# Kernel tuning notes

Hardware: AMD Instinct MI355X
Metric: run time of the kernel (lower is better)

Reference implementation:

```python
import jax, jax.numpy as jnp
import numpy as np

N = 100000      # nodes
E = 1600000     # edges
F_IN = 512      # num_features
H = 128         # hidden
C = 40          # num_classes
K = 10          # Chebyshev order


def setup_inputs() -> dict:
    key = jax.random.key(0)
    ks = jax.random.split(key, 6)
    x = jax.random.normal(ks[0], (N, F_IN), dtype=jnp.float32)
    edge_index = jax.random.randint(ks[1], (2, E), 0, N, dtype=jnp.int32)
    W1 = jax.random.normal(ks[2], (F_IN, H), dtype=jnp.float32) / np.sqrt(F_IN).astype(np.float32)
    b1 = jnp.zeros((H,), dtype=jnp.float32)
    W2 = jax.random.normal(ks[3], (H, C), dtype=jnp.float32) / np.sqrt(H).astype(np.float32)
    b2 = jnp.zeros((C,), dtype=jnp.float32)
    # Chebyshev coefficients temp[K+1]
    temp = 1.0 + 0.1 * jax.random.normal(ks[4], (K + 1,), dtype=jnp.float32)
    return {"x": x, "edge_index": edge_index, "W1": W1, "b1": b1, "W2": W2, "b2": b2, "temp": temp}


def reference(x, edge_index, W1, b1, W2, b2, temp):
    # MLP encoder (eval mode: dropout is identity)
    h = jax.nn.relu(x @ W1 + b1)          # [N, H]
    h = h @ W2 + b2                        # [N, C]

    # gcn_norm: add self-loops, symmetric normalization
    self_loop = jnp.arange(N, dtype=edge_index.dtype)
    row = jnp.concatenate([edge_index[0], self_loop])   # [E+N]
    col = jnp.concatenate([edge_index[1], self_loop])
    deg = jax.ops.segment_sum(jnp.ones_like(row, dtype=jnp.float32), row, num_segments=N)
    dis = jnp.where(deg > 0, jax.lax.rsqrt(jnp.maximum(deg, 1.0)), 0.0)
    norm = dis[row] * dis[col]             # [E+N]

    def prop(v):  # A_hat @ v : gather-scale-scatter over edges
        return jax.ops.segment_sum(norm[:, None] * v[col], row, num_segments=N)

    # Chebyshev recurrence: Tx_k = 2*A_hat*Tx_{k-1} - Tx_{k-2}
    Tx0 = h
    Tx1 = prop(h)
    out0 = temp[0] * Tx0 + temp[1] * Tx1

    def body(carry, coe):
        t0, t1, acc = carry
        t2 = 2.0 * prop(t1) - t0
        return (t1, t2, acc + coe * t2), None

    (_, _, out), _ = jax.lax.scan(body, (Tx0, Tx1, out0), temp[2:])
    return jax.nn.log_softmax(out, axis=1)
```

## Files before the change

### kernel.cpp

```cpp
#include <hip/hip_runtime.h>
#include <hip/hip_bf16.h>
#include <cstdint>
#include <cstddef>

#define NN   100000
#define EE   1600000
#define FIN  512
#define HID  128
#define CC   40
#define KORD 10
#define SHB  80
#define SHSTRIDE ((size_t)NN * SHB)

typedef __attribute__((ext_vector_type(4))) float f4;
typedef __attribute__((ext_vector_type(8))) short short8_t;
typedef __attribute__((ext_vector_type(4))) unsigned int u4;
typedef __attribute__((ext_vector_type(4), aligned(4))) int i4u;

__device__ __forceinline__ unsigned short cvt_bf16(float f) {
  union { float f; unsigned u; } a; a.f = f;
  unsigned r = a.u + 0x7fffu + ((a.u >> 16) & 1u);
  return (unsigned short)(r >> 16);
}
__device__ __forceinline__ unsigned pk_bf(float a, float b) {
  union { float f; unsigned u; } x, y; x.f = a; y.f = b;
  unsigned ra = x.u + 0x7fffu + ((x.u >> 16) & 1u);
  unsigned rb = y.u + 0x7fffu + ((y.u >> 16) & 1u);
  return (ra >> 16) | (rb & 0xffff0000u);
}
__device__ __forceinline__ unsigned pk_tr(float a, float b) {
  union { float f; unsigned u; } x, y; x.f = a; y.f = b;
  return (x.u >> 16) | (y.u & 0xffff0000u);
}
__device__ __forceinline__ f4 cvf2(unsigned lo, unsigned hi) {
  union { unsigned u; float f; } a, b, c, d;
  a.u = lo << 16; b.u = lo & 0xffff0000u;
  c.u = hi << 16; d.u = hi & 0xffff0000u;
  f4 r; r.x = a.f; r.y = b.f; r.z = c.f; r.w = d.f; return r;
}

__global__ __launch_bounds__(256) void k_dw(const int* __restrict__ rowI, int* __restrict__ deg,
                                            const float* __restrict__ W1, unsigned short* __restrict__ W1T,
                                            int ndeg) {
  int b = blockIdx.x;
  if (b < ndeg) {
    int i = b * 256 + threadIdx.x;
    if (i < EE) atomicAdd(&deg[rowI[i]], 1);
  } else {
    int idx = (b - ndeg) * 256 + threadIdx.x;
    int k = idx >> 7, n = idx & 127;
    W1T[(k >> 5) * 4096 + n * 32 + (k & 31)] = cvt_bf16(W1[idx]);
  }
}

__global__ __launch_bounds__(256) void k_scan1(const int* __restrict__ cnt, int* __restrict__ excl,
                                               int* __restrict__ bsums) {
  __shared__ int s[256];
  int tid = threadIdx.x;
  int base = blockIdx.x * 1024 + tid * 4;
  int v0 = (base + 0 < NN) ? cnt[base + 0] + 1 : 0;
  int v1 = (base + 1 < NN) ? cnt[base + 1] + 1 : 0;
  int v2 = (base + 2 < NN) ? cnt[base + 2] + 1 : 0;
  int v3 = (base + 3 < NN) ? cnt[base + 3] + 1 : 0;
  int tsum = v0 + v1 + v2 + v3;
  s[tid] = tsum;
  __syncthreads();
  for (int off = 1; off < 256; off <<= 1) {
    int t = (tid >= off) ? s[tid - off] : 0;
    __syncthreads();
    if (tid >= off) s[tid] += t;
    __syncthreads();
  }
  int run = s[tid] - tsum;
  if (tid == 255) bsums[blockIdx.x] = s[255];
  if (base + 0 < NN) excl[base + 0] = run; run += v0;
  if (base + 1 < NN) excl[base + 1] = run; run += v1;
  if (base + 2 < NN) excl[base + 2] = run; run += v2;
  if (base + 3 < NN) excl[base + 3] = run;
}

__global__ __launch_bounds__(128) void k_scan2(int* __restrict__ bsums, int nb) {
  __shared__ int s[128];
  int tid = threadIdx.x;
  int v = (tid < nb) ? bsums[tid] : 0;
  s[tid] = v;
  __syncthreads();
  for (int off = 1; off < 128; off <<= 1) {
    int t = (tid >= off) ? s[tid - off] : 0;
    __syncthreads();
    if (tid >= off) s[tid] += t;
    __syncthreads();
  }
  if (tid < nb) bsums[tid] = s[tid] - v;
}

__global__ __launch_bounds__(256) void k_scan3(const int* __restrict__ cnt, int* __restrict__ rs,
                                               int* __restrict__ cur, const int* __restrict__ bsums,
                                               float* __restrict__ dis, float* __restrict__ sqd,
                                               float* __restrict__ invd) {
  int i = blockIdx.x * 256 + threadIdx.x;
  if (i < NN) {
    int v = rs[i] + bsums[i >> 10];
    rs[i] = v;
    cur[i] = v;
    int d = cnt[i] + 1;
    if (i == NN - 1) rs[NN] = v + d;
    float fd = (float)d;
    dis[i]  = rsqrtf(fd);
    sqd[i]  = sqrtf(fd);
    invd[i] = 1.0f / fd;
  }
}

#define SLICE_ROWS (NN / 8)
#define SC_CHUNK   2048
__global__ __launch_bounds__(256) void k_scatter(const int* __restrict__ rowI, const int* __restrict__ colI,
                                                 int* __restrict__ cur, int* __restrict__ colS) {
  int slice = blockIdx.x & 7;
  int chunk = blockIdx.x >> 3;
  int lo = slice * SLICE_ROWS, hi = lo + SLICE_ROWS;
#pragma unroll
  for (int t = 0; t < SC_CHUNK / 256; ++t) {
    int i = chunk * SC_CHUNK + t * 256 + threadIdx.x;
    if (i < EE + NN) {
      int r = (i < EE) ? rowI[i] : (i - EE);
      if (r >= lo && r < hi) {
        int c = (i < EE) ? colI[i] : r;
        int pos = atomicAdd(&cur[r], 1);
        colS[pos] = c * SHB;
      }
    }
  }
}

#define LDK 40
__global__ __launch_bounds__(256) void k_gemm1(const float* __restrict__ x, const unsigned short* __restrict__ W1T,
                                               const float* __restrict__ b1, float* __restrict__ h1) {
  __shared__ __align__(16) float As_f[128 * 32];
  __shared__ __align__(16) short Bs_s[128][LDK];
  int tid  = threadIdx.x;
  int wave = tid >> 6, lane = tid & 63;
  int blockRow = blockIdx.x * 128;
  int wr = (wave & 1) * 64, wc = (wave >> 1) * 64;
  int l15 = lane & 15, hi4 = lane >> 4;

  int sr = (wave << 5) + (lane >> 3);
  int sslot = lane & 7;

  f4 acc[4][4] = {};

  for (int k0 = 0; k0 < FIN; k0 += 32) {
#pragma unroll
    for (int c = 0; c < 4; ++c) {
      int row = sr + c * 8;
      int gr = blockRow + row;
      int lslot = sslot ^ (row & 7);
      const float* gp = x + (size_t)gr * FIN + k0 + lslot * 4;
      float* lp = &As_f[(wave << 10) + (c << 8)];
      if (gr < NN) {
        __builtin_amdgcn_global_load_lds(
            (const __attribute__((address_space(1))) unsigned int*)gp,
            (__attribute__((address_space(3))) unsigned int*)lp, 16, 0, 0);
      }
    }

    const unsigned short* Wt = W1T + (k0 >> 5) * 4096;
    short8_t q0 = *(const short8_t*)&Wt[tid * 16];
    short8_t q1 = *(const short8_t*)&Wt[tid * 16 + 8];
    int bn = tid >> 1, bkk = (tid & 1) * 16;
    *(short8_t*)&Bs_s[bn][bkk]     = q0;
    *(short8_t*)&Bs_s[bn][bkk + 8] = q1;

    __syncthreads();

    short8_t afr[4], bfr[4];
#pragma unroll
    for (int m = 0; m < 4; ++m) {
      int row = wr + m * 16 + l15;
      int s0 = (hi4 * 2) ^ (row & 7);
      int s1 = (hi4 * 2 + 1) ^ (row & 7);
      f4 a0 = *(const f4*)&As_f[(row << 5) + s0 * 4];
      f4 a1 = *(const f4*)&As_f[(row << 5) + s1 * 4];
      u4 p;
      p.x = pk_tr(a0.x, a0.y); p.y = pk_tr(a0.z, a0.w);
      p.z = pk_tr(a1.x, a1.y); p.w = pk_tr(a1.z, a1.w);
      afr[m] = *(short8_t*)&p;
    }
#pragma unroll
    for (int n = 0; n < 4; ++n) bfr[n] = *(const short8_t*)&Bs_s[wc + n * 16 + l15][hi4 * 8];
#pragma unroll
    for (int m = 0; m < 4; ++m)
#pragma unroll
      for (int n = 0; n < 4; ++n)
        acc[m][n] = __builtin_amdgcn_mfma_f32_16x16x32_bf16(afr[m], bfr[n], acc[m][n], 0, 0, 0);

    __syncthreads();
  }

  float bias[4];
#pragma unroll
  for (int n = 0; n < 4; ++n) bias[n] = b1[wc + n * 16 + l15];
#pragma unroll
  for (int m = 0; m < 4; ++m) {
    int baseRow = blockRow + wr + m * 16 + hi4 * 4;
#pragma unroll
    for (int n = 0; n < 4; ++n) {
      int col = wc + n * 16 + l15;
#pragma unroll
      for (int r = 0; r < 4; ++r) {
        int grow = baseRow + r;
        if (grow < NN) h1[(size_t)grow * HID + col] = fmaxf(acc[m][n][r] + bias[n], 0.f);
      }
    }
  }
}

__global__ __launch_bounds__(256) void k_gemm2(const float* __restrict__ h1, const float* __restrict__ W2,
                                               const float* __restrict__ b2, const float* __restrict__ temp,
                                               const float* __restrict__ dis,
                                               unsigned short* __restrict__ sh0) {
  __shared__ float sW[HID * CC];
  __shared__ float sb[CC];
  int tid = threadIdx.x;
  for (int i = tid; i < HID * CC; i += 256) sW[i] = W2[i];
  if (tid < CC) sb[tid] = b2[tid];
  __syncthreads();
  int gid = blockIdx.x * 256 + tid;
  if (gid >= NN * 20) return;
  int row = gid / 20;
  int c2  = (gid - row * 20) * 2;
  const float* hr = h1 + (size_t)row * HID;
  float a0 = sb[c2], a1 = sb[c2 + 1];
#pragma unroll 8
  for (int k = 0; k < HID; ++k) {
    float hv = hr[k];
    a0 = fmaf(hv, sW[k * CC + c2], a0);
    a1 = fmaf(hv, sW[k * CC + c2 + 1], a1);
  }
  float dv = dis[row];
  *(unsigned*)((char*)sh0 + (size_t)row * SHB + c2 * 2) = pk_bf(a0 * dv, a1 * dv);
}

template <int MODE>
__global__ __launch_bounds__(256, 8) void k_prop(const unsigned short* __restrict__ shIn,
                                                 const unsigned short* __restrict__ shPrev,
                                                 unsigned short* __restrict__ shOut,
                                                 const int* __restrict__ colS,
                                                 const int* __restrict__ rs,
                                                 const float* __restrict__ invd) {
  int lane = threadIdx.x & 63;
  int wave = threadIdx.x >> 6;
  int grp  = lane / 5;
  int fi   = lane - grp * 5;
  int node = blockIdx.x * 48 + wave * 12 + grp;
  bool active = (grp < 12) && (node < NN);
  int s = 0, e = 0;
  if (active) { s = rs[node]; e = rs[node + 1]; }
  const char* base = (const char*)shIn + fi * 16;
  f4 z = {0.f, 0.f, 0.f, 0.f};
  f4 alo0 = z, ahi0 = z, alo1 = z, ahi1 = z;
  int j = s;
  for (; j + 4 <= e; j += 4) {
    i4u c = *(const i4u*)&colS[j];
    u4 p0 = *(const u4*)(base + c.x);
    u4 p1 = *(const u4*)(base + c.y);
    u4 p2 = *(const u4*)(base + c.z);
    u4 p3 = *(const u4*)(base + c.w);
    alo0 += cvf2(p0.x, p0.y); ahi0 += cvf2(p0.z, p0.w);
    alo1 += cvf2(p1.x, p1.y); ahi1 += cvf2(p1.z, p1.w);
    alo0 += cvf2(p2.x, p2.y); ahi0 += cvf2(p2.z, p2.w);
    alo1 += cvf2(p3.x, p3.y); ahi1 += cvf2(p3.z, p3.w);
  }
  if (j + 2 <= e) {
    u4 p0 = *(const u4*)(base + colS[j]);
    u4 p1 = *(const u4*)(base + colS[j + 1]);
    alo0 += cvf2(p0.x, p0.y); ahi0 += cvf2(p0.z, p0.w);
    alo1 += cvf2(p1.x, p1.y); ahi1 += cvf2(p1.z, p1.w);
    j += 2;
  }
  if (j < e) {
    u4 p0 = *(const u4*)(base + colS[j]);
    alo0 += cvf2(p0.x, p0.y); ahi0 += cvf2(p0.z, p0.w);
  }

  if (active) {
    f4 slo = alo0 + alo1;
    f4 shi = ahi0 + ahi1;
    float iv = invd[node];
    size_t ro = (size_t)node * SHB + fi * 16;
    f4 wlo, whi;
    if (MODE == 0) {
      wlo = iv * slo; whi = iv * shi;
    } else {
      u4 pp = __builtin_nontemporal_load((const u4*)((const char*)shPrev + ro));
      f4 plo = cvf2(pp.x, pp.y), phi = cvf2(pp.z, pp.w);
      wlo = (2.f * iv) * slo - plo;
      whi = (2.f * iv) * shi - phi;
    }
    u4 pk;
    pk.x = pk_bf(wlo.x, wlo.y); pk.y = pk_bf(wlo.z, wlo.w);
    pk.z = pk_bf(whi.x, whi.y); pk.w = pk_bf(whi.z, whi.w);
    *(u4*)((char*)shOut + ro) = pk;
  }
}

__global__ __launch_bounds__(256) void k_comb(const unsigned short* __restrict__ shBase,
                                              float* __restrict__ outF,
                                              const float* __restrict__ sqd,
                                              const float* __restrict__ temp) {
  int lane = threadIdx.x & 63;
  int wave = threadIdx.x >> 6;
  int grp  = lane / 5;
  int fi   = lane - grp * 5;
  int node = blockIdx.x * 48 + wave * 12 + grp;
  if (grp >= 12 || node >= NN) return;

  const char* p = (const char*)shBase + (size_t)node * SHB + fi * 16;
  f4 alo = {0.f,0.f,0.f,0.f}, ahi = alo;
#pragma unroll
  for (int k = 0; k <= KORD; ++k) {
    u4 pp = *(const u4*)(p + (size_t)k * SHSTRIDE);
    float tk = temp[k];
    alo += tk * cvf2(pp.x, pp.y);
    ahi += tk * cvf2(pp.z, pp.w);
  }
  float sq = sqd[node];
  alo *= sq; ahi *= sq;

  int gb = grp * 5;
  float m = fmaxf(fmaxf(fmaxf(alo.x, alo.y), fmaxf(alo.z, alo.w)),
                  fmaxf(fmaxf(ahi.x, ahi.y), fmaxf(ahi.z, ahi.w)));
  float mm = m;
#pragma unroll
  for (int j = 0; j < 5; ++j) mm = fmaxf(mm, __shfl(m, gb + j));
  float ss = expf(alo.x - mm) + expf(alo.y - mm) + expf(alo.z - mm) + expf(alo.w - mm)
           + expf(ahi.x - mm) + expf(ahi.y - mm) + expf(ahi.z - mm) + expf(ahi.w - mm);
  float tot = 0.f;
#pragma unroll
  for (int j = 0; j < 5; ++j) tot += __shfl(ss, gb + j);
  float lse = mm + logf(tot);
  alo -= lse; ahi -= lse;
  size_t o = (size_t)node * CC + fi * 8;
  *(f4*)&outF[o]     = alo;
  *(f4*)&outF[o + 4] = ahi;
}

extern "C" void kernel_launch(void* const* d_in, const int* in_sizes, int n_in,
                              void* d_out, int out_size, void* d_ws, size_t ws_size,
                              hipStream_t stream) {
  const float* x    = (const float*)d_in[0];
  const int*   ei   = (const int*)d_in[1];
  const float* W1   = (const float*)d_in[2];
  const float* b1   = (const float*)d_in[3];
  const float* W2   = (const float*)d_in[4];
  const float* b2   = (const float*)d_in[5];
  const float* temp = (const float*)d_in[6];
  const int* rowI = ei;
  const int* colI = ei + EE;
  float* out = (float*)d_out;

  char* w = (char*)d_ws;
  auto alloc = [&](size_t bytes) -> void* {
    void* p = (void*)w;
    w += (bytes + 255) & ~(size_t)255;
    return p;
  };
  int*   deg   = (int*)  alloc((size_t)NN * 4);
  float* dis   = (float*)alloc((size_t)NN * 4);
  float* sqd   = (float*)alloc((size_t)NN * 4);
  float* invd  = (float*)alloc((size_t)NN * 4);
  int*   rs    = (int*)  alloc((size_t)(NN + 1) * 4);
  int*   cur   = (int*)  alloc((size_t)NN * 4);
  int*   bsums = (int*)  alloc(512 * 4);
  unsigned short* W1T = (unsigned short*)alloc((size_t)FIN * HID * 2);
  unsigned short* shAll = (unsigned short*)alloc(SHSTRIDE * (KORD + 1));
  int*   colS  = (int*)  alloc((size_t)(EE + NN) * 4);
  float* h1    = (float*)alloc((size_t)NN * HID * 4);

  auto sh = [&](int k) -> unsigned short* {
    return (unsigned short*)((char*)shAll + (size_t)k * SHSTRIDE);
  };

  hipMemsetAsync(deg, 0, (size_t)NN * 4, stream);

  const int NDEG = (EE + 255) / 256;
  const int NW1T = FIN * HID / 256;
  k_dw<<<NDEG + NW1T, 256, 0, stream>>>(rowI, deg, W1, W1T, NDEG);

  int nb = (NN + 1023) / 1024;
  k_scan1<<<nb, 256, 0, stream>>>(deg, rs, bsums);
  k_scan2<<<1, 128, 0, stream>>>(bsums, nb);
  k_scan3<<<(NN + 255) / 256, 256, 0, stream>>>(deg, rs, cur, bsums, dis, sqd, invd);

  const int NCH = (EE + NN + SC_CHUNK - 1) / SC_CHUNK;
  k_scatter<<<8 * NCH, 256, 0, stream>>>(rowI, colI, cur, colS);

  k_gemm1<<<(NN + 127) / 128, 256, 0, stream>>>(x, W1T, b1, h1);
  k_gemm2<<<(NN * 20 + 255) / 256, 256, 0, stream>>>(h1, W2, b2, temp, dis, sh(0));

  int G = (NN + 47) / 48;
  k_prop<0><<<G, 256, 0, stream>>>(sh(0), sh(0), sh(1), colS, rs, invd);
  for (int k = 2; k <= KORD; ++k) {
    k_prop<1><<<G, 256, 0, stream>>>(sh(k - 1), sh(k - 2), sh(k), colS, rs, invd);
  }

  k_comb<<<(NN + 47) / 48, 256, 0, stream>>>(shAll, out, sqd, temp);
}
```

Measured before the change: 631.9 us.

## Sort nodes by degree for load-balanced propagation and pad feature rows

Adds a degree histogram and counting sort that builds a permutation of nodes ordered by degree. The propagation kernels then process nodes in this order, so the groups within a wave have similar edge counts and lanes sit idle less. The per-node feature stride also grows from 80 to 128 bytes, which aligns rows but raises memory footprint and gather traffic. Node processing order becomes scattered, which may hurt write locality.

```diff
diff --git a/kernel.cpp b/kernel.cpp
--- a/kernel.cpp
+++ b/kernel.cpp
@@ -9,7 +9,7 @@
 #define HID  128
 #define CC   40
 #define KORD 10
-#define SHB  80
+#define SHB  128
 #define SHSTRIDE ((size_t)NN * SHB)
 
 typedef __attribute__((ext_vector_type(4))) float f4;
@@ -54,14 +54,18 @@
 }
 
 __global__ __launch_bounds__(256) void k_scan1(const int* __restrict__ cnt, int* __restrict__ excl,
-                                               int* __restrict__ bsums) {
+                                               int* __restrict__ bsums, int* __restrict__ hist) {
   __shared__ int s[256];
+  __shared__ int lh[256];
   int tid = threadIdx.x;
+  lh[tid] = 0;
+  __syncthreads();
   int base = blockIdx.x * 1024 + tid * 4;
-  int v0 = (base + 0 < NN) ? cnt[base + 0] + 1 : 0;
-  int v1 = (base + 1 < NN) ? cnt[base + 1] + 1 : 0;
-  int v2 = (base + 2 < NN) ? cnt[base + 2] + 1 : 0;
-  int v3 = (base + 3 < NN) ? cnt[base + 3] + 1 : 0;
+  int v0 = 0, v1 = 0, v2 = 0, v3 = 0;
+  if (base + 0 < NN) { v0 = cnt[base + 0] + 1; atomicAdd(&lh[min(v0, 255)], 1); }
+  if (base + 1 < NN) { v1 = cnt[base + 1] + 1; atomicAdd(&lh[min(v1, 255)], 1); }
+  if (base + 2 < NN) { v2 = cnt[base + 2] + 1; atomicAdd(&lh[min(v2, 255)], 1); }
+  if (base + 3 < NN) { v3 = cnt[base + 3] + 1; atomicAdd(&lh[min(v3, 255)], 1); }
   int tsum = v0 + v1 + v2 + v3;
   s[tid] = tsum;
   __syncthreads();
@@ -77,38 +81,63 @@
   if (base + 1 < NN) excl[base + 1] = run; run += v1;
   if (base + 2 < NN) excl[base + 2] = run; run += v2;
   if (base + 3 < NN) excl[base + 3] = run;
-}
-
-__global__ __launch_bounds__(128) void k_scan2(int* __restrict__ bsums, int nb) {
-  __shared__ int s[128];
+  if (lh[tid] > 0) atomicAdd(&hist[tid], lh[tid]);
+}
+
+__global__ __launch_bounds__(256) void k_scan2h(int* __restrict__ bsums, int nb, int* __restrict__ hist) {
+  __shared__ int s[256];
   int tid = threadIdx.x;
-  int v = (tid < nb) ? bsums[tid] : 0;
+  int* arr = (blockIdx.x == 0) ? bsums : hist;
+  int lim  = (blockIdx.x == 0) ? nb : 256;
+  int v = (tid < lim) ? arr[tid] : 0;
   s[tid] = v;
   __syncthreads();
-  for (int off = 1; off < 128; off <<= 1) {
+  for (int off = 1; off < 256; off <<= 1) {
     int t = (tid >= off) ? s[tid - off] : 0;
     __syncthreads();
     if (tid >= off) s[tid] += t;
     __syncthreads();
   }
-  if (tid < nb) bsums[tid] = s[tid] - v;
-}
-
-__global__ __launch_bounds__(256) void k_scan3(const int* __restrict__ cnt, int* __restrict__ rs,
-                                               int* __restrict__ cur, const int* __restrict__ bsums,
-                                               float* __restrict__ dis, float* __restrict__ sqd,
-                                               float* __restrict__ invd) {
-  int i = blockIdx.x * 256 + threadIdx.x;
-  if (i < NN) {
-    int v = rs[i] + bsums[i >> 10];
-    rs[i] = v;
-    cur[i] = v;
-    int d = cnt[i] + 1;
-    if (i == NN - 1) rs[NN] = v + d;
-    float fd = (float)d;
-    dis[i]  = rsqrtf(fd);
-    sqd[i]  = sqrtf(fd);
-    invd[i] = 1.0f / fd;
+  if (tid < lim) arr[tid] = s[tid] - v;
+}
+
+__global__ __launch_bounds__(256) void k_scan3p(const int* __restrict__ cnt, int* __restrict__ rs,
+                                                int* __restrict__ cur, const int* __restrict__ bsums,
+                                                float* __restrict__ dis, float* __restrict__ sqd,
+                                                float* __restrict__ invd,
+                                                const int* __restrict__ hoff, int* __restrict__ gcur,
+                                                int* __restrict__ perm, int nb3) {
+  int b = blockIdx.x;
+  int tid = threadIdx.x;
+  if (b < nb3) {
+    int i = b * 256 + tid;
+    if (i < NN) {
+      int v = rs[i] + bsums[i >> 10];
+      rs[i] = v;
+      cur[i] = v;
+      int d = cnt[i] + 1;
+      if (i == NN - 1) rs[NN] = v + d;
+      float fd = (float)d;
+      dis[i]  = rsqrtf(fd);
+      sqd[i]  = sqrtf(fd);
+      invd[i] = 1.0f / fd;
+    }
+  } else {
+    __shared__ int lh[256];
+    __shared__ int lb[256];
+    lh[tid] = 0;
+    __syncthreads();
+    int i = (b - nb3) * 256 + tid;
+    int d = 0, rank = 0;
+    bool ok = (i < NN);
+    if (ok) {
+      d = min(cnt[i] + 1, 255);
+      rank = atomicAdd(&lh[d], 1);
+    }
+    __syncthreads();
+    if (lh[tid] > 0) lb[tid] = atomicAdd(&gcur[tid], lh[tid]);
+    __syncthreads();
+    if (ok) perm[hoff[d] + lb[d] + rank] = i;
   }
 }
 
@@ -247,15 +276,16 @@
                                                  unsigned short* __restrict__ shOut,
                                                  const int* __restrict__ colS,
                                                  const int* __restrict__ rs,
+                                                 const int* __restrict__ perm,
                                                  const float* __restrict__ invd) {
   int lane = threadIdx.x & 63;
   int wave = threadIdx.x >> 6;
   int grp  = lane / 5;
   int fi   = lane - grp * 5;
-  int node = blockIdx.x * 48 + wave * 12 + grp;
-  bool active = (grp < 12) && (node < NN);
-  int s = 0, e = 0;
-  if (active) { s = rs[node]; e = rs[node + 1]; }
+  int nidx = blockIdx.x * 48 + wave * 12 + grp;
+  bool active = (grp < 12) && (nidx < NN);
+  int node = 0, s = 0, e = 0;
+  if (active) { node = perm[nidx]; s = rs[node]; e = rs[node + 1]; }
   const char* base = (const char*)shIn + fi * 16;
   f4 z = {0.f, 0.f, 0.f, 0.f};
   f4 alo0 = z, ahi0 = z, alo1 = z, ahi1 = z;
@@ -371,7 +401,10 @@
   float* invd  = (float*)alloc((size_t)NN * 4);
   int*   rs    = (int*)  alloc((size_t)(NN + 1) * 4);
   int*   cur   = (int*)  alloc((size_t)NN * 4);
+  int*   perm  = (int*)  alloc((size_t)NN * 4);
   int*   bsums = (int*)  alloc(512 * 4);
+  int*   hist  = (int*)  alloc(256 * 4);
+  int*   gcur  = (int*)  alloc(256 * 4);
   unsigned short* W1T = (unsigned short*)alloc((size_t)FIN * HID * 2);
   unsigned short* shAll = (unsigned short*)alloc(SHSTRIDE * (KORD + 1));
   int*   colS  = (int*)  alloc((size_t)(EE + NN) * 4);
@@ -382,15 +415,18 @@
   };
 
   hipMemsetAsync(deg, 0, (size_t)NN * 4, stream);
+  hipMemsetAsync(hist, 0, 256 * 4, stream);
+  hipMemsetAsync(gcur, 0, 256 * 4, stream);
 
   const int NDEG = (EE + 255) / 256;
   const int NW1T = FIN * HID / 256;
   k_dw<<<NDEG + NW1T, 256, 0, stream>>>(rowI, deg, W1, W1T, NDEG);
 
   int nb = (NN + 1023) / 1024;
-  k_scan1<<<nb, 256, 0, stream>>>(deg, rs, bsums);
-  k_scan2<<<1, 128, 0, stream>>>(bsums, nb);
-  k_scan3<<<(NN + 255) / 256, 256, 0, stream>>>(deg, rs, cur, bsums, dis, sqd, invd);
+  k_scan1<<<nb, 256, 0, stream>>>(deg, rs, bsums, hist);
+  k_scan2h<<<2, 256, 0, stream>>>(bsums, nb, hist);
+  int nb3 = (NN + 255) / 256;
+  k_scan3p<<<2 * nb3, 256, 0, stream>>>(deg, rs, cur, bsums, dis, sqd, invd, hist, gcur, perm, nb3);
 
   const int NCH = (EE + NN + SC_CHUNK - 1) / SC_CHUNK;
   k_scatter<<<8 * NCH, 256, 0, stream>>>(rowI, colI, cur, colS);
@@ -399,9 +435,9 @@
   k_gemm2<<<(NN * 20 + 255) / 256, 256, 0, stream>>>(h1, W2, b2, temp, dis, sh(0));
 
   int G = (NN + 47) / 48;
-  k_prop<0><<<G, 256, 0, stream>>>(sh(0), sh(0), sh(1), colS, rs, invd);
+  k_prop<0><<<G, 256, 0, stream>>>(sh(0), sh(0), sh(1), colS, rs, perm, invd);
   for (int k = 2; k <= KORD; ++k) {
-    k_prop<1><<<G, 256, 0, stream>>>(sh(k - 1), sh(k - 2), sh(k), colS, rs, invd);
+    k_prop<1><<<G, 256, 0, stream>>>(sh(k - 1), sh(k - 2), sh(k), colS, rs, perm, invd);
   }
 
   k_comb<<<(NN + 47) / 48, 256, 0, stream>>>(shAll, out, sqd, temp);
```

Result: slower. 678.1 us (+7.3%).

## Split propagation features into two column halves with separate node-major planes

Applied to the files above, without the earlier changes.

Stores each Chebyshev feature buffer as two 40-byte-per-node planes (first and second 20 classes) instead of one 80-byte row, and launches the propagation kernel over both halves with twice the blocks. Each half-plane is 4 MB instead of 8 MB, so the working set of the random gathers in each half-pass is smaller and more likely to stay cache-resident. Each gather becomes an 8-byte load instead of 16 bytes. In exchange, the edge list and row pointers are read twice per propagation step, and more, smaller memory transactions are issued.

```diff
diff --git a/kernel.cpp b/kernel.cpp
--- a/kernel.cpp
+++ b/kernel.cpp
@@ -9,12 +9,13 @@
 #define HID  128
 #define CC   40
 #define KORD 10
-#define SHB  80
-#define SHSTRIDE ((size_t)NN * SHB)
+#define HBYTES ((size_t)NN * 40)
+#define SHSTRIDE ((size_t)NN * 80)
 
 typedef __attribute__((ext_vector_type(4))) float f4;
 typedef __attribute__((ext_vector_type(8))) short short8_t;
 typedef __attribute__((ext_vector_type(4))) unsigned int u4;
+typedef __attribute__((ext_vector_type(2))) unsigned int u2;
 typedef __attribute__((ext_vector_type(4), aligned(4))) int i4u;
 
 __device__ __forceinline__ unsigned short cvt_bf16(float f) {
@@ -127,7 +128,7 @@
       if (r >= lo && r < hi) {
         int c = (i < EE) ? colI[i] : r;
         int pos = atomicAdd(&cur[r], 1);
-        colS[pos] = c * SHB;
+        colS[pos] = c * 40;
       }
     }
   }
@@ -238,7 +239,9 @@
     a1 = fmaf(hv, sW[k * CC + c2 + 1], a1);
   }
   float dv = dis[row];
-  *(unsigned*)((char*)sh0 + (size_t)row * SHB + c2 * 2) = pk_bf(a0 * dv, a1 * dv);
+  size_t ro = (c2 < 20) ? ((size_t)row * 40 + c2 * 2)
+                        : (HBYTES + (size_t)row * 40 + (c2 - 20) * 2);
+  *(unsigned*)((char*)sh0 + ro) = pk_bf(a0 * dv, a1 * dv);
 }
 
 template <int MODE>
@@ -247,60 +250,59 @@
                                                  unsigned short* __restrict__ shOut,
                                                  const int* __restrict__ colS,
                                                  const int* __restrict__ rs,
-                                                 const float* __restrict__ invd) {
+                                                 const float* __restrict__ invd, int GP) {
+  int b = blockIdx.x;
+  size_t half = 0;
+  if (b >= GP) { half = HBYTES; b -= GP; }
   int lane = threadIdx.x & 63;
   int wave = threadIdx.x >> 6;
   int grp  = lane / 5;
   int fi   = lane - grp * 5;
-  int node = blockIdx.x * 48 + wave * 12 + grp;
+  int node = b * 48 + wave * 12 + grp;
   bool active = (grp < 12) && (node < NN);
   int s = 0, e = 0;
   if (active) { s = rs[node]; e = rs[node + 1]; }
-  const char* base = (const char*)shIn + fi * 16;
+  const char* base = (const char*)shIn + half + fi * 8;
   f4 z = {0.f, 0.f, 0.f, 0.f};
-  f4 alo0 = z, ahi0 = z, alo1 = z, ahi1 = z;
+  f4 a0 = z, a1 = z, a2 = z, a3 = z;
   int j = s;
   for (; j + 4 <= e; j += 4) {
     i4u c = *(const i4u*)&colS[j];
-    u4 p0 = *(const u4*)(base + c.x);
-    u4 p1 = *(const u4*)(base + c.y);
-    u4 p2 = *(const u4*)(base + c.z);
-    u4 p3 = *(const u4*)(base + c.w);
-    alo0 += cvf2(p0.x, p0.y); ahi0 += cvf2(p0.z, p0.w);
-    alo1 += cvf2(p1.x, p1.y); ahi1 += cvf2(p1.z, p1.w);
-    alo0 += cvf2(p2.x, p2.y); ahi0 += cvf2(p2.z, p2.w);
-    alo1 += cvf2(p3.x, p3.y); ahi1 += cvf2(p3.z, p3.w);
+    u2 p0 = *(const u2*)(base + c.x);
+    u2 p1 = *(const u2*)(base + c.y);
+    u2 p2 = *(const u2*)(base + c.z);
+    u2 p3 = *(const u2*)(base + c.w);
+    a0 += cvf2(p0.x, p0.y);
+    a1 += cvf2(p1.x, p1.y);
+    a2 += cvf2(p2.x, p2.y);
+    a3 += cvf2(p3.x, p3.y);
   }
   if (j + 2 <= e) {
-    u4 p0 = *(const u4*)(base + colS[j]);
-    u4 p1 = *(const u4*)(base + colS[j + 1]);
-    alo0 += cvf2(p0.x, p0.y); ahi0 += cvf2(p0.z, p0.w);
-    alo1 += cvf2(p1.x, p1.y); ahi1 += cvf2(p1.z, p1.w);
+    u2 p0 = *(const u2*)(base + colS[j]);
+    u2 p1 = *(const u2*)(base + colS[j + 1]);
+    a0 += cvf2(p0.x, p0.y);
+    a1 += cvf2(p1.x, p1.y);
     j += 2;
   }
   if (j < e) {
-    u4 p0 = *(const u4*)(base + colS[j]);
-    alo0 += cvf2(p0.x, p0.y); ahi0 += cvf2(p0.z, p0.w);
+    u2 p0 = *(const u2*)(base + colS[j]);
+    a2 += cvf2(p0.x, p0.y);
   }
 
   if (active) {
-    f4 slo = alo0 + alo1;
-    f4 shi = ahi0 + ahi1;
+    f4 sum = (a0 + a1) + (a2 + a3);
     float iv = invd[node];
-    size_t ro = (size_t)node * SHB + fi * 16;
-    f4 wlo, whi;
+    size_t ro = half + (size_t)node * 40 + fi * 8;
+    f4 wv;
     if (MODE == 0) {
-      wlo = iv * slo; whi = iv * shi;
+      wv = iv * sum;
     } else {
-      u4 pp = __builtin_nontemporal_load((const u4*)((const char*)shPrev + ro));
-      f4 plo = cvf2(pp.x, pp.y), phi = cvf2(pp.z, pp.w);
-      wlo = (2.f * iv) * slo - plo;
-      whi = (2.f * iv) * shi - phi;
+      u2 pp = __builtin_nontemporal_load((const u2*)((const char*)shPrev + ro));
+      wv = (2.f * iv) * sum - cvf2(pp.x, pp.y);
     }
-    u4 pk;
-    pk.x = pk_bf(wlo.x, wlo.y); pk.y = pk_bf(wlo.z, wlo.w);
-    pk.z = pk_bf(whi.x, whi.y); pk.w = pk_bf(whi.z, whi.w);
-    *(u4*)((char*)shOut + ro) = pk;
+    u2 pk;
+    pk.x = pk_bf(wv.x, wv.y); pk.y = pk_bf(wv.z, wv.w);
+    *(u2*)((char*)shOut + ro) = pk;
   }
 }
 
@@ -315,14 +317,16 @@
   int node = blockIdx.x * 48 + wave * 12 + grp;
   if (grp >= 12 || node >= NN) return;
 
-  const char* p = (const char*)shBase + (size_t)node * SHB + fi * 16;
+  const char* p0 = (const char*)shBase + (size_t)node * 40 + fi * 8;
+  const char* p1 = p0 + HBYTES;
   f4 alo = {0.f,0.f,0.f,0.f}, ahi = alo;
 #pragma unroll
   for (int k = 0; k <= KORD; ++k) {
-    u4 pp = *(const u4*)(p + (size_t)k * SHSTRIDE);
+    u2 qa = *(const u2*)(p0 + (size_t)k * SHSTRIDE);
+    u2 qb = *(const u2*)(p1 + (size_t)k * SHSTRIDE);
     float tk = temp[k];
-    alo += tk * cvf2(pp.x, pp.y);
-    ahi += tk * cvf2(pp.z, pp.w);
+    alo += tk * cvf2(qa.x, qa.y);
+    ahi += tk * cvf2(qb.x, qb.y);
   }
   float sq = sqd[node];
   alo *= sq; ahi *= sq;
@@ -340,9 +344,9 @@
   for (int j = 0; j < 5; ++j) tot += __shfl(ss, gb + j);
   float lse = mm + logf(tot);
   alo -= lse; ahi -= lse;
-  size_t o = (size_t)node * CC + fi * 8;
-  *(f4*)&outF[o]     = alo;
-  *(f4*)&outF[o + 4] = ahi;
+  size_t o = (size_t)node * CC;
+  *(f4*)&outF[o + fi * 4]       = alo;
+  *(f4*)&outF[o + 20 + fi * 4]  = ahi;
 }
 
 extern "C" void kernel_launch(void* const* d_in, const int* in_sizes, int n_in,
@@ -398,11 +402,11 @@
   k_gemm1<<<(NN + 127) / 128, 256, 0, stream>>>(x, W1T, b1, h1);
   k_gemm2<<<(NN * 20 + 255) / 256, 256, 0, stream>>>(h1, W2, b2, temp, dis, sh(0));
 
-  int G = (NN + 47) / 48;
-  k_prop<0><<<G, 256, 0, stream>>>(sh(0), sh(0), sh(1), colS, rs, invd);
+  int GP = (NN + 47) / 48;
+  k_prop<0><<<2 * GP, 256, 0, stream>>>(sh(0), sh(0), sh(1), colS, rs, invd, GP);
   for (int k = 2; k <= KORD; ++k) {
-    k_prop<1><<<G, 256, 0, stream>>>(sh(k - 1), sh(k - 2), sh(k), colS, rs, invd);
-  }
-
-  k_comb<<<(NN + 47) / 48, 256, 0, stream>>>(shAll, out, sqd, temp);
-}
+    k_prop<1><<<2 * GP, 256, 0, stream>>>(sh(k - 1), sh(k - 2), sh(k), colS, rs, invd, GP);
+  }
+
+  k_comb<<<GP, 256, 0, stream>>>(shAll, out, sqd, temp);
+}
```

New measurement: 660.6 us. 1.05x slower.
